# Performance work log

Hardware: AMD Instinct MI355X
Metric: run time of the kernel (lower is better)

The kernel has to match this reference:

```python
import jax, jax.numpy as jnp
import numpy as np

B, N, T, C = 2, 2048, 32, 32
NUM_BASES, MAX_K, K_CURR = 4, 32, 16


def setup_inputs() -> dict:
    key = jax.random.key(0)
    k1, k2, k3, k4, k5 = jax.random.split(key, 5)
    z = jax.random.normal(k1, (B, N, T, C), dtype=jnp.float32)
    neighbor_indices = jax.random.randint(k2, (N, K_CURR), 0, N)
    # parameters (match torch init scales)
    adjacency = 0.5 + 0.01 * jax.random.normal(k3, (N, MAX_K), dtype=jnp.float32)
    basis_weights = 0.02 * jax.random.normal(k4, (NUM_BASES, N, MAX_K), dtype=jnp.float32)
    channel_coeffs = jax.random.normal(k5, (C, NUM_BASES), dtype=jnp.float32)
    return {
        "z": z,
        "neighbor_indices": neighbor_indices,
        "adjacency": adjacency,
        "basis_weights": basis_weights,
        "channel_coeffs": channel_coeffs,
    }


def reference(z, neighbor_indices, adjacency, basis_weights, channel_coeffs):
    # z: [B,N,T,C], neighbor_indices: [N,k]
    k = neighbor_indices.shape[1]
    bases = basis_weights[:, :, :k]        # [num_bases, N, k]
    adj = adjacency[:, :k]                 # [N, k]
    # per-channel effective edge weights: [C, N, k]
    eff = jnp.einsum('cb,bnk->cnk', channel_coeffs, bases)
    edge_w = eff * adj[None, :, :]         # [C, N, k]
    w = jnp.transpose(edge_w, (1, 2, 0))   # [N, k, C]
    # gather neighbor features: [B, N, k, T, C]
    z_neigh = z[:, neighbor_indices]
    # weighted sum over neighbors, per-channel weights
    out = jnp.einsum('bnktc,nkc->bntc', z_neigh, w)
    return jnp.tanh(out)
```

## Files before the change

### kernel.cpp

```cpp
#include <hip/hip_runtime.h>


constexpr int BB_    = 2;
constexpr int NN_    = 2048;
constexpr int TT_    = 32;
constexpr int CC_    = 32;
constexpr int NBASE_ = 4;
constexpr int MAXK_  = 32;
constexpr int KC_    = 16;

constexpr int TQ_      = 4;
constexpr int NODES_PB = 4;
constexpr int PLANE_   = TT_ * CC_;
constexpr int SLICE_   = (TT_ / TQ_) * CC_;

__device__ __forceinline__ float fast_tanh(float x) {
    float e = __expf(2.0f * x);
    float r = __builtin_amdgcn_rcpf(e + 1.0f);
    return fmaf(-2.0f, r, 1.0f);
}

__device__ __forceinline__ unsigned pack_bf16(float x, float y) {
    unsigned ux = __float_as_uint(x), uy = __float_as_uint(y);
    ux = (ux + 0x7fffu + ((ux >> 16) & 1u)) >> 16;
    uy = (uy + 0x7fffu + ((uy >> 16) & 1u)) >> 16;
    return ux | (uy << 16);
}
__device__ __forceinline__ float blo(unsigned u) { return __uint_as_float(u << 16); }
__device__ __forceinline__ float bhi(unsigned u) { return __uint_as_float(u & 0xffff0000u); }

__global__ __launch_bounds__(256) void z_to_bf16(
    const float4* __restrict__ z4, uint4* __restrict__ zb)
{
    const int gid = blockIdx.x * 256 + threadIdx.x;
    float4 a = z4[2 * gid];
    float4 b = z4[2 * gid + 1];
    zb[gid] = make_uint4(pack_bf16(a.x, a.y), pack_bf16(a.z, a.w),
                         pack_bf16(b.x, b.y), pack_bf16(b.z, b.w));
}

__global__ __launch_bounds__(256, 4) void cgl_kernel(
    const unsigned short* __restrict__ zb,
    const int*   __restrict__ nbr,
    const float* __restrict__ adj,
    const float* __restrict__ bw,
    const float* __restrict__ cc,
    float*       __restrict__ out)
{
    __shared__ __align__(16) float w_s[NODES_PB][KC_][CC_];
    __shared__ float bw_s[NODES_PB][NBASE_][KC_];
    __shared__ float cc_s[NBASE_][CC_];
    __shared__ float adj_s[NODES_PB][KC_];

    const int tid = threadIdx.x;
    const int blk = blockIdx.x;

    const int xcd   = blk & 7;
    const int b     = xcd >> 2;
    const int tq    = xcd & 3;
    const int group = blk >> 3;
    const int node0 = group * NODES_PB;

    {
        int nd = tid >> 6, bb = (tid >> 4) & 3, k = tid & 15;
        bw_s[nd][bb][k] = bw[((size_t)bb * NN_ + (node0 + nd)) * MAXK_ + k];

        if (tid < 64) {
            int nd2 = tid >> 4, k2 = tid & 15;
            adj_s[nd2][k2] = adj[(size_t)(node0 + nd2) * MAXK_ + k2];
        } else if (tid < 192) {
            int i = tid - 64, bb2 = i >> 5, c2 = i & 31;
            cc_s[bb2][c2] = cc[c2 * NBASE_ + bb2];
        }
    }

    const int wave = tid >> 6;
    const int lane = tid & 63;
    const int n    = node0 + wave;
    const int* __restrict__ ip = nbr + n * KC_;
    int nks[KC_];
    #pragma unroll
    for (int k = 0; k < KC_; ++k)
        nks[k] = __builtin_amdgcn_readfirstlane(ip[k]);

    __syncthreads();

    {
        int i = tid;
        #pragma unroll
        for (int r = 0; r < 8; ++r, i += 256) {
            int nd = i >> 9, k = (i >> 5) & 15, c = i & 31;
            float s = cc_s[0][c] * bw_s[nd][0][k]
                    + cc_s[1][c] * bw_s[nd][1][k]
                    + cc_s[2][c] * bw_s[nd][2][k]
                    + cc_s[3][c] * bw_s[nd][3][k];
            w_s[nd][k][c] = s * adj_s[nd][k];
        }
    }

    uint2 zv[KC_];
    {
        const size_t sbase = (size_t)b * NN_ * PLANE_ + (size_t)tq * SLICE_;
        #pragma unroll
        for (int k = 0; k < KC_; ++k) {
            const unsigned short* row = zb + sbase + (size_t)nks[k] * PLANE_;
            zv[k] = ((const uint2*)row)[lane];
        }
    }

    __syncthreads();

    const int c0 = (lane & 7) << 2;
    float4 acc = make_float4(0.f, 0.f, 0.f, 0.f);
    #pragma unroll
    for (int k = 0; k < KC_; ++k) {
        float4 wv = *(const float4*)&w_s[wave][k][c0];
        acc.x = fmaf(blo(zv[k].x), wv.x, acc.x);
        acc.y = fmaf(bhi(zv[k].x), wv.y, acc.y);
        acc.z = fmaf(blo(zv[k].y), wv.z, acc.z);
        acc.w = fmaf(bhi(zv[k].y), wv.w, acc.w);
    }

    float4 o;
    o.x = fast_tanh(acc.x);
    o.y = fast_tanh(acc.y);
    o.z = fast_tanh(acc.z);
    o.w = fast_tanh(acc.w);

    float* op = out + ((size_t)(b * NN_ + n) * TT_ + tq * (TT_ / TQ_)) * CC_;
    ((float4*)op)[lane] = o;
}

extern "C" void kernel_launch(void* const* d_in, const int* in_sizes, int n_in,
                              void* d_out, int out_size, void* d_ws, size_t ws_size,
                              hipStream_t stream) {
    const float* z   = (const float*)d_in[0];
    const int*   nbr = (const int*)d_in[1];
    const float* adj = (const float*)d_in[2];
    const float* bw  = (const float*)d_in[3];
    const float* cc  = (const float*)d_in[4];
    float* out = (float*)d_out;
    unsigned short* zb16 = (unsigned short*)d_ws;

    z_to_bf16<<<dim3(BB_ * NN_ * PLANE_ / 8 / 256), dim3(256), 0, stream>>>(
        (const float4*)z, (uint4*)zb16);
    cgl_kernel<<<dim3(BB_ * TQ_ * (NN_ / NODES_PB)), dim3(256), 0, stream>>>(
        zb16, nbr, adj, bw, cc, out);
}
```

Measured before the change: 90.82 us.

## Drop bf16 pre-conversion pass and gather fp32 z directly, issuing loads early

Removes the separate z_to_bf16 kernel, so each gather reads fp32 z straight from the input and no longer needs a second launch or a full read-and-write pass over z. The neighbor-index reads and the 16 float4 gathers now start before the shared-memory weight setup, so their latency overlaps that work. In exchange each gather moves twice as many bytes as the bf16 version, and each thread holds 16 float4 values, which raises register pressure. It also restores full fp32 accuracy for z.

Result: faster. 87.82 us (-3.3%).

```diff
diff --git a/kernel.cpp b/kernel.cpp
--- a/kernel.cpp
+++ b/kernel.cpp
@@ -11,8 +11,8 @@
 
 constexpr int TQ_      = 4;
 constexpr int NODES_PB = 4;
-constexpr int PLANE_   = TT_ * CC_;
-constexpr int SLICE_   = (TT_ / TQ_) * CC_;
+constexpr int PLANE4_  = TT_ * CC_ / 4;
+constexpr int SLICE4_  = (TT_ / TQ_) * CC_ / 4;
 
 __device__ __forceinline__ float fast_tanh(float x) {
     float e = __expf(2.0f * x);
@@ -20,27 +20,8 @@
     return fmaf(-2.0f, r, 1.0f);
 }
 
-__device__ __forceinline__ unsigned pack_bf16(float x, float y) {
-    unsigned ux = __float_as_uint(x), uy = __float_as_uint(y);
-    ux = (ux + 0x7fffu + ((ux >> 16) & 1u)) >> 16;
-    uy = (uy + 0x7fffu + ((uy >> 16) & 1u)) >> 16;
-    return ux | (uy << 16);
-}
-__device__ __forceinline__ float blo(unsigned u) { return __uint_as_float(u << 16); }
-__device__ __forceinline__ float bhi(unsigned u) { return __uint_as_float(u & 0xffff0000u); }
-
-__global__ __launch_bounds__(256) void z_to_bf16(
-    const float4* __restrict__ z4, uint4* __restrict__ zb)
-{
-    const int gid = blockIdx.x * 256 + threadIdx.x;
-    float4 a = z4[2 * gid];
-    float4 b = z4[2 * gid + 1];
-    zb[gid] = make_uint4(pack_bf16(a.x, a.y), pack_bf16(a.z, a.w),
-                         pack_bf16(b.x, b.y), pack_bf16(b.z, b.w));
-}
-
 __global__ __launch_bounds__(256, 4) void cgl_kernel(
-    const unsigned short* __restrict__ zb,
+    const float* __restrict__ z,
     const int*   __restrict__ nbr,
     const float* __restrict__ adj,
     const float* __restrict__ bw,
@@ -61,6 +42,25 @@
     const int group = blk >> 3;
     const int node0 = group * NODES_PB;
 
+    const int wave = tid >> 6;
+    const int lane = tid & 63;
+    const int n    = node0 + wave;
+
+    const int* __restrict__ ip = nbr + n * KC_;
+    int nks[KC_];
+    #pragma unroll
+    for (int k = 0; k < KC_; ++k)
+        nks[k] = __builtin_amdgcn_readfirstlane(ip[k]);
+
+    float4 zv[KC_];
+    {
+        const float4* __restrict__ z4 =
+            (const float4*)z + (size_t)b * NN_ * PLANE4_ + (size_t)tq * SLICE4_ + lane;
+        #pragma unroll
+        for (int k = 0; k < KC_; ++k)
+            zv[k] = z4[(size_t)nks[k] * PLANE4_];
+    }
+
     {
         int nd = tid >> 6, bb = (tid >> 4) & 3, k = tid & 15;
         bw_s[nd][bb][k] = bw[((size_t)bb * NN_ + (node0 + nd)) * MAXK_ + k];
@@ -73,16 +73,6 @@
             cc_s[bb2][c2] = cc[c2 * NBASE_ + bb2];
         }
     }
-
-    const int wave = tid >> 6;
-    const int lane = tid & 63;
-    const int n    = node0 + wave;
-    const int* __restrict__ ip = nbr + n * KC_;
-    int nks[KC_];
-    #pragma unroll
-    for (int k = 0; k < KC_; ++k)
-        nks[k] = __builtin_amdgcn_readfirstlane(ip[k]);
-
     __syncthreads();
 
     {
@@ -97,28 +87,17 @@
             w_s[nd][k][c] = s * adj_s[nd][k];
         }
     }
-
-    uint2 zv[KC_];
-    {
-        const size_t sbase = (size_t)b * NN_ * PLANE_ + (size_t)tq * SLICE_;
-        #pragma unroll
-        for (int k = 0; k < KC_; ++k) {
-            const unsigned short* row = zb + sbase + (size_t)nks[k] * PLANE_;
-            zv[k] = ((const uint2*)row)[lane];
-        }
-    }
-
     __syncthreads();
 
-    const int c0 = (lane & 7) << 2;
+    const int c0 = (lane << 2) & 31;
     float4 acc = make_float4(0.f, 0.f, 0.f, 0.f);
     #pragma unroll
     for (int k = 0; k < KC_; ++k) {
         float4 wv = *(const float4*)&w_s[wave][k][c0];
-        acc.x = fmaf(blo(zv[k].x), wv.x, acc.x);
-        acc.y = fmaf(bhi(zv[k].x), wv.y, acc.y);
-        acc.z = fmaf(blo(zv[k].y), wv.z, acc.z);
-        acc.w = fmaf(bhi(zv[k].y), wv.w, acc.w);
+        acc.x = fmaf(zv[k].x, wv.x, acc.x);
+        acc.y = fmaf(zv[k].y, wv.y, acc.y);
+        acc.z = fmaf(zv[k].z, wv.z, acc.z);
+        acc.w = fmaf(zv[k].w, wv.w, acc.w);
     }
 
     float4 o;
@@ -127,8 +106,8 @@
     o.z = fast_tanh(acc.z);
     o.w = fast_tanh(acc.w);
 
-    float* op = out + ((size_t)(b * NN_ + n) * TT_ + tq * (TT_ / TQ_)) * CC_;
-    ((float4*)op)[lane] = o;
+    float4* op = (float4*)out + (size_t)(b * NN_ + n) * PLANE4_ + tq * SLICE4_;
+    op[lane] = o;
 }
 
 extern "C" void kernel_launch(void* const* d_in, const int* in_sizes, int n_in,
@@ -140,10 +119,7 @@
     const float* bw  = (const float*)d_in[3];
     const float* cc  = (const float*)d_in[4];
     float* out = (float*)d_out;
-    unsigned short* zb16 = (unsigned short*)d_ws;
 
-    z_to_bf16<<<dim3(BB_ * NN_ * PLANE_ / 8 / 256), dim3(256), 0, stream>>>(
-        (const float4*)z, (uint4*)zb16);
     cgl_kernel<<<dim3(BB_ * TQ_ * (NN_ / NODES_PB)), dim3(256), 0, stream>>>(
-        zb16, nbr, adj, bw, cc, out);
+        z, nbr, adj, bw, cc, out);
 }
```
